# Kernel optimization log

Measured on AMD Instinct MI355X. Metric: run time of the kernel, lower is better.

Reference implementation:

```python
import jax, jax.numpy as jnp
import numpy as np

EPS = 1e-5
LEAK = 0.33  # scn LeakyReLU default leakiness


def leaky(x):
    return jnp.where(x > 0, x, LEAK * x)


def subm_conv(feat, idx, mask, w):
    # feat: [N,C], idx: [N,K] int, mask: [N,K] bool, w: [K,Cin,Cout]
    g = feat[idx] * mask[..., None]          # [N,K,C] gather of active neighbors
    return jnp.einsum('nkc,kcd->nd', g, w)   # [N,Cout]


def batch_norm(x, gamma, beta):
    # scn BatchNormalization in training mode: batch stats over active sites
    m = x.mean(axis=0)
    v = x.var(axis=0)
    return (x - m) * jax.lax.rsqrt(v + EPS) * gamma + beta


def setup_inputs() -> dict:
    key = jax.random.key(0)
    ks = jax.random.split(key, 8)
    N, K, C, B = 131072, 9, 64, 4
    features = jax.random.normal(ks[0], (N, C), dtype=jnp.float32)
    neighbor_idx = jax.random.randint(ks[1], (N, K), 0, N, dtype=jnp.int32)
    # center offset always points at self (submanifold conv semantics)
    neighbor_idx = neighbor_idx.at[:, K // 2].set(jnp.arange(N, dtype=jnp.int32))
    neighbor_mask = jax.random.randint(ks[2], (N, K), 0, 2) > 0
    neighbor_mask = neighbor_mask.at[:, K // 2].set(True)
    scale = 1.0 / np.sqrt(K * C)
    conv1_w = jax.random.normal(ks[3], (B, K, C, C), dtype=jnp.float32) * scale
    conv2_w = jax.random.normal(ks[4], (B, K, C, C), dtype=jnp.float32) * scale
    bn1_gamma = jnp.ones((B, C), dtype=jnp.float32)
    bn1_beta = jnp.zeros((B, C), dtype=jnp.float32)
    bn2_gamma = jnp.ones((B, C), dtype=jnp.float32)
    bn2_beta = jnp.zeros((B, C), dtype=jnp.float32)
    return {
        'features': features, 'neighbor_idx': neighbor_idx, 'neighbor_mask': neighbor_mask,
        'conv1_w': conv1_w, 'bn1_gamma': bn1_gamma, 'bn1_beta': bn1_beta,
        'conv2_w': conv2_w, 'bn2_gamma': bn2_gamma, 'bn2_beta': bn2_beta,
    }


def reference(features, neighbor_idx, neighbor_mask, conv1_w, bn1_gamma, bn1_beta,
              conv2_w, bn2_gamma, bn2_beta):
    x = features
    n_blocks = conv1_w.shape[0]
    for b in range(n_blocks):
        residual = x
        out = subm_conv(x, neighbor_idx, neighbor_mask, conv1_w[b])
        out = leaky(batch_norm(out, bn1_gamma[b], bn1_beta[b]))
        out = subm_conv(out, neighbor_idx, neighbor_mask, conv2_w[b])
        out = batch_norm(out, bn2_gamma[b], bn2_beta[b])
        x = leaky(out + residual)
    return x
```

## Files before the change

kernel.cpp:

```cpp
#include <hip/hip_runtime.h>
#include <hip/hip_bf16.h>
#include <stdint.h>

#define NROWS 131072
#define EPSBN 1e-5f
#define LEAKK 0.33f

typedef __bf16 bf16x8_t __attribute__((ext_vector_type(8)));
typedef float  f32x4_t  __attribute__((ext_vector_type(4)));

__device__ __forceinline__ float leaky_f(float x) { return fmaxf(x, LEAKK * x); }

#define GLDS16(g, l)                                                          \
    __builtin_amdgcn_global_load_lds(                                         \
        (const __attribute__((address_space(1))) void*)(g),                   \
        (__attribute__((address_space(3))) void*)(l), 16, 0, 0)

#define WAIT_VM18 0x4F72
#define WAIT_VM10 0x0F7A
#define WAIT_VM8  0x0F78
#define WAIT_VM0  0x0F70
#define CFENCE() asm volatile("" ::: "memory")

__global__ __launch_bounds__(256, 2) void conv_kernel(
    const __bf16* __restrict__ src,
    const int* __restrict__ cidxT,
    const __bf16* __restrict__ wt,
    __bf16* __restrict__ dst,
    float* __restrict__ stat_out)
{
    __shared__ char Ab[2][32768];
    __shared__ char Bb[2][8192];

    const int tid  = threadIdx.x;
    const int lane = tid & 63;
    const int wv   = tid >> 6;
    const int quad = lane >> 4;
    const int l15  = lane & 15;
    const int row0 = blockIdx.x << 8;
    const int srow = tid >> 3;
    const int cg   = (tid & 7) ^ (srow & 7);
    const int ldsl = (tid & 192) << 4;
    const int sxor = l15 & 7;

    const char* srcb = (const char*)src;
    const char* wtb  = (const char*)wt;

    f32x4_t acc[4][4];
#pragma unroll
    for (int mt = 0; mt < 4; ++mt)
#pragma unroll
        for (int nt = 0; nt < 4; ++nt)
            acc[mt][nt] = (f32x4_t){0.f, 0.f, 0.f, 0.f};

    int ix[2][8];
#pragma unroll
    for (int i = 0; i < 8; ++i) ix[0][i] = cidxT[row0 + (i << 5) + srow];
    CFENCE();
#pragma unroll
    for (int i = 0; i < 8; ++i) ix[1][i] = cidxT[NROWS + row0 + (i << 5) + srow];
    CFENCE();
    __builtin_amdgcn_s_waitcnt(WAIT_VM8);
#pragma unroll
    for (int i = 0; i < 8; ++i)
        GLDS16(srcb + ((size_t)ix[0][i] << 7) + (cg << 4), &Ab[0][(i << 12) + ldsl]);
#pragma unroll
    for (int i = 0; i < 2; ++i)
        GLDS16(wtb + (((i << 5) + srow) << 7) + (cg << 4), &Bb[0][(i << 12) + ldsl]);
    CFENCE();

#pragma unroll
    for (int k = 0; k < 9; ++k) {
        const int cur = k & 1, nxt = cur ^ 1;
        if (k < 7) {
#pragma unroll
            for (int i = 0; i < 8; ++i)
                ix[k & 1][i] = cidxT[(k + 2) * NROWS + row0 + (i << 5) + srow];
        }
        CFENCE();
        if (k < 7)       __builtin_amdgcn_s_waitcnt(WAIT_VM18);
        else if (k == 7) __builtin_amdgcn_s_waitcnt(WAIT_VM10);
        if (k < 8) {
            const int* ixu = ix[(k + 1) & 1];
#pragma unroll
            for (int i = 0; i < 8; ++i)
                GLDS16(srcb + ((size_t)ixu[i] << 7) + (cg << 4),
                       &Ab[nxt][(i << 12) + ldsl]);
#pragma unroll
            for (int i = 0; i < 2; ++i)
                GLDS16(wtb + ((size_t)(k + 1) << 13) + (((i << 5) + srow) << 7) + (cg << 4),
                       &Bb[nxt][(i << 12) + ldsl]);
        }
        CFENCE();
        if (k < 7)       __builtin_amdgcn_s_waitcnt(WAIT_VM18);
        else if (k == 7) __builtin_amdgcn_s_waitcnt(WAIT_VM10);
        else             __builtin_amdgcn_s_waitcnt(WAIT_VM0);
        __builtin_amdgcn_s_barrier();
        bf16x8_t af[4][2], bq[4][2];
#pragma unroll
        for (int ks = 0; ks < 2; ++ks) {
            const int slot = ((quad | (ks << 2)) ^ sxor) << 4;
#pragma unroll
            for (int mt = 0; mt < 4; ++mt) {
                int m = (wv << 6) + (mt << 4) + l15;
                af[mt][ks] = *(const bf16x8_t*)&Ab[cur][(m << 7) + slot];
            }
#pragma unroll
            for (int nt = 0; nt < 4; ++nt) {
                int d = (nt << 4) + l15;
                bq[nt][ks] = *(const bf16x8_t*)&Bb[cur][(d << 7) + slot];
            }
        }
#pragma unroll
        for (int ks = 0; ks < 2; ++ks)
#pragma unroll
            for (int mt = 0; mt < 4; ++mt)
#pragma unroll
                for (int nt = 0; nt < 4; ++nt)
                    acc[mt][nt] = __builtin_amdgcn_mfma_f32_16x16x32_bf16(
                        af[mt][ks], bq[nt][ks], acc[mt][nt], 0, 0, 0);
        __builtin_amdgcn_s_barrier();
    }

#pragma unroll
    for (int mt = 0; mt < 4; ++mt) {
        int rowb = row0 + (wv << 6) + (mt << 4) + (quad << 2);
#pragma unroll
        for (int nt = 0; nt < 4; ++nt) {
            int col = (nt << 4) + l15;
#pragma unroll
            for (int r = 0; r < 4; ++r)
                dst[((size_t)(rowb + r) << 6) + col] = (__bf16)acc[mt][nt][r];
        }
    }
    float* red = (float*)Bb[1];
    __syncthreads();
    if (tid < 128) red[tid] = 0.f;
    __syncthreads();
#pragma unroll
    for (int nt = 0; nt < 4; ++nt) {
        float s = 0.f, q = 0.f;
#pragma unroll
        for (int mt = 0; mt < 4; ++mt)
#pragma unroll
            for (int r = 0; r < 4; ++r) { float v = acc[mt][nt][r]; s += v; q += v * v; }
        s += __shfl_xor(s, 16); s += __shfl_xor(s, 32);
        q += __shfl_xor(q, 16); q += __shfl_xor(q, 32);
        if (lane < 16) {
            atomicAdd(&red[(nt << 4) + lane], s);
            atomicAdd(&red[64 + (nt << 4) + lane], q);
        }
    }
    __syncthreads();
    if (tid < 128) atomicAdd(&stat_out[tid], red[tid]);
}

__global__ __launch_bounds__(256) void bnact_kernel(
    __bf16* __restrict__ y, const float* __restrict__ stat,
    const float* __restrict__ gamma, const float* __restrict__ beta)
{
    __shared__ float sc[64], sh[64];
    int tid = threadIdx.x;
    if (tid < 64) {
        float m = stat[tid] * (1.f / NROWS);
        float v = stat[64 + tid] * (1.f / NROWS) - m * m;
        float s = gamma[tid] * rsqrtf(v + EPSBN);
        sc[tid] = s;
        sh[tid] = beta[tid] - m * s;
    }
    __syncthreads();
    size_t base = ((((size_t)blockIdx.x << 8) | tid) << 3);
    int c0 = (int)(base & 63);
    bf16x8_t hv = *(bf16x8_t*)(y + base);
#pragma unroll
    for (int j = 0; j < 8; ++j) {
        float f = (float)hv[j];
        f = leaky_f(f * sc[c0 + j] + sh[c0 + j]);
        hv[j] = (__bf16)f;
    }
    *(bf16x8_t*)(y + base) = hv;
}

__global__ __launch_bounds__(256) void resid_kernel(
    const __bf16* __restrict__ z, const float* __restrict__ xin,
    float* __restrict__ xf, __bf16* __restrict__ xh, float* __restrict__ dout,
    const float* __restrict__ stat, const float* __restrict__ gamma,
    const float* __restrict__ beta, int isfinal)
{
    __shared__ float sc[64], sh[64];
    int tid = threadIdx.x;
    if (tid < 64) {
        float m = stat[tid] * (1.f / NROWS);
        float v = stat[64 + tid] * (1.f / NROWS) - m * m;
        float s = gamma[tid] * rsqrtf(v + EPSBN);
        sc[tid] = s;
        sh[tid] = beta[tid] - m * s;
    }
    __syncthreads();
    size_t base = ((((size_t)blockIdx.x << 8) | tid) << 3);
    int c0 = (int)(base & 63);
    bf16x8_t zv = *(const bf16x8_t*)(z + base);
    float4 xa = *(const float4*)(xin + base);
    float4 xb = *(const float4*)(xin + base + 4);
    float o[8];
#pragma unroll
    for (int j = 0; j < 8; ++j) {
        float xv = (j < 4) ? (&xa.x)[j] : (&xb.x)[j - 4];
        o[j] = leaky_f((float)zv[j] * sc[c0 + j] + sh[c0 + j] + xv);
    }
    if (isfinal) {
        *(float4*)(dout + base)     = make_float4(o[0], o[1], o[2], o[3]);
        *(float4*)(dout + base + 4) = make_float4(o[4], o[5], o[6], o[7]);
    } else {
        *(float4*)(xf + base)     = make_float4(o[0], o[1], o[2], o[3]);
        *(float4*)(xf + base + 4) = make_float4(o[4], o[5], o[6], o[7]);
        bf16x8_t h;
#pragma unroll
        for (int j = 0; j < 8; ++j) h[j] = (__bf16)o[j];
        *(bf16x8_t*)(xh + base) = h;
    }
}

__global__ __launch_bounds__(256) void prep_kernel(
    const float* __restrict__ feat, const float* __restrict__ w1,
    const float* __restrict__ w2, const int* __restrict__ nidx,
    const unsigned char* __restrict__ mraw,
    __bf16* __restrict__ fh, __bf16* __restrict__ yh,
    __bf16* __restrict__ wtp, int* __restrict__ cidxT,
    float* __restrict__ stats)
{
    size_t t = ((size_t)blockIdx.x << 8) | threadIdx.x;
    if (t < 1024) stats[t] = 0.f;
    if (t < 64) {
        fh[(size_t)NROWS * 64 + t] = (__bf16)0.f;
        yh[(size_t)NROWS * 64 + t] = (__bf16)0.f;
    }
    if (t < 1048576) {
        size_t i = t << 3;
        float4 a = *(const float4*)(feat + i);
        float4 b = *(const float4*)(feat + i + 4);
        bf16x8_t h;
        h[0] = (__bf16)a.x; h[1] = (__bf16)a.y; h[2] = (__bf16)a.z; h[3] = (__bf16)a.w;
        h[4] = (__bf16)b.x; h[5] = (__bf16)b.y; h[6] = (__bf16)b.z; h[7] = (__bf16)b.w;
        *(bf16x8_t*)(fh + i) = h;
    }
    if (t < 294912) {
        int o = (int)t;
        int c = o & 63, d = (o >> 6) & 63;
        int kk = o >> 12;
        int k = kk % 9, bb = (kk / 9) & 3, cv = kk / 36;
        const float* w = cv ? w2 : w1;
        float v = w[((size_t)((bb * 9 + k) * 64 + c) << 6) + d];
        wtp[o] = (__bf16)v;
    }
    if (t < 1179648) {
        int k = (int)(t >> 17), n = (int)(t & 131071);
        bool bytes_enc = (mraw[13] != 0);
        int e = n * 9 + k;
        bool m = bytes_enc ? (mraw[e] != 0) : (((const unsigned int*)mraw)[e] != 0u);
        cidxT[t] = m ? nidx[e] : NROWS;
    }
}

extern "C" void kernel_launch(void* const* d_in, const int* in_sizes, int n_in,
                              void* d_out, int out_size, void* d_ws, size_t ws_size,
                              hipStream_t stream) {
    const float* feat = (const float*)d_in[0];
    const int* nidx = (const int*)d_in[1];
    const unsigned char* mraw = (const unsigned char*)d_in[2];
    const float* w1 = (const float*)d_in[3];
    const float* g1 = (const float*)d_in[4];
    const float* b1 = (const float*)d_in[5];
    const float* w2 = (const float*)d_in[6];
    const float* g2 = (const float*)d_in[7];
    const float* b2 = (const float*)d_in[8];
    float* out = (float*)d_out;

    char* ws = (char*)d_ws;
    float*  xf    = (float*)ws;
    __bf16* xh    = (__bf16*)(ws + 33554432);
    __bf16* yh    = (__bf16*)(ws + 50331904);
    __bf16* zh    = (__bf16*)(ws + 67109376);
    __bf16* wtp   = (__bf16*)(ws + 83886592);
    float*  stats = (float*)(ws + 84476416);
    int*    cidxT = (int*)(ws + 84480512);

    prep_kernel<<<4608, 256, 0, stream>>>(feat, w1, w2, nidx, mraw,
                                          xh, yh, wtp, cidxT, stats);

    for (int b = 0; b < 4; ++b) {
        conv_kernel<<<512, 256, 0, stream>>>(
            xh, cidxT, wtp + (size_t)b * 9 * 4096,
            yh, stats + (size_t)(2 * b) * 128);
        bnact_kernel<<<4096, 256, 0, stream>>>(
            yh, stats + (size_t)(2 * b) * 128, g1 + b * 64, b1 + b * 64);
        conv_kernel<<<512, 256, 0, stream>>>(
            yh, cidxT, wtp + (size_t)(4 + b) * 9 * 4096,
            zh, stats + (size_t)(2 * b + 1) * 128);
        resid_kernel<<<4096, 256, 0, stream>>>(
            zh, (b == 0) ? feat : xf, xf, xh, out,
            stats + (size_t)(2 * b + 1) * 128, g2 + b * 64, b2 + b * 64,
            (b == 3) ? 1 : 0);
    }
}
```

Before: 418.2 us.

## Drop fp32 residual buffer, restructure conv waits, and coalesce index prep

The fp32 residual copy xf is removed, so the residual kernel reads the bf16 activation xh in place and no longer writes fp32 state. This halves residual traffic at the cost of bf16 rounding on the residual path. The conv loop drops the early vmcnt wait before issuing the next gathers and instead adds an lgkm wait before the closing barrier. The prep kernel now handles one row per thread across all 9 offsets, with a smaller grid.

```diff
diff --git a/kernel.cpp b/kernel.cpp
--- a/kernel.cpp
+++ b/kernel.cpp
@@ -16,10 +16,11 @@
         (const __attribute__((address_space(1))) void*)(g),                   \
         (__attribute__((address_space(3))) void*)(l), 16, 0, 0)
 
-#define WAIT_VM18 0x4F72
-#define WAIT_VM10 0x0F7A
-#define WAIT_VM8  0x0F78
-#define WAIT_VM0  0x0F70
+#define WAIT_VM18  0x4F72
+#define WAIT_VM10  0x0F7A
+#define WAIT_VM8   0x0F78
+#define WAIT_VM0   0x0F70
+#define WAIT_LGKM0 0xC07F
 #define CFENCE() asm volatile("" ::: "memory")
 
 __global__ __launch_bounds__(256, 2) void conv_kernel(
@@ -78,8 +79,6 @@
                 ix[k & 1][i] = cidxT[(k + 2) * NROWS + row0 + (i << 5) + srow];
         }
         CFENCE();
-        if (k < 7)       __builtin_amdgcn_s_waitcnt(WAIT_VM18);
-        else if (k == 7) __builtin_amdgcn_s_waitcnt(WAIT_VM10);
         if (k < 8) {
             const int* ixu = ix[(k + 1) & 1];
 #pragma unroll
@@ -119,7 +118,10 @@
                 for (int nt = 0; nt < 4; ++nt)
                     acc[mt][nt] = __builtin_amdgcn_mfma_f32_16x16x32_bf16(
                         af[mt][ks], bq[nt][ks], acc[mt][nt], 0, 0, 0);
+        CFENCE();
+        __builtin_amdgcn_s_waitcnt(WAIT_LGKM0);
         __builtin_amdgcn_s_barrier();
+        CFENCE();
     }
 
 #pragma unroll
@@ -182,10 +184,10 @@
 }
 
 __global__ __launch_bounds__(256) void resid_kernel(
-    const __bf16* __restrict__ z, const float* __restrict__ xin,
-    float* __restrict__ xf, __bf16* __restrict__ xh, float* __restrict__ dout,
+    const __bf16* __restrict__ z, const float* __restrict__ featin,
+    __bf16* __restrict__ xh, float* __restrict__ dout,
     const float* __restrict__ stat, const float* __restrict__ gamma,
-    const float* __restrict__ beta, int isfinal)
+    const float* __restrict__ beta, int isfirst, int isfinal)
 {
     __shared__ float sc[64], sh[64];
     int tid = threadIdx.x;
@@ -200,20 +202,25 @@
     size_t base = ((((size_t)blockIdx.x << 8) | tid) << 3);
     int c0 = (int)(base & 63);
     bf16x8_t zv = *(const bf16x8_t*)(z + base);
-    float4 xa = *(const float4*)(xin + base);
-    float4 xb = *(const float4*)(xin + base + 4);
+    float xv[8];
+    if (isfirst) {
+        float4 xa = *(const float4*)(featin + base);
+        float4 xb = *(const float4*)(featin + base + 4);
+#pragma unroll
+        for (int j = 0; j < 4; ++j) { xv[j] = (&xa.x)[j]; xv[4 + j] = (&xb.x)[j]; }
+    } else {
+        bf16x8_t xr = *(const bf16x8_t*)(xh + base);
+#pragma unroll
+        for (int j = 0; j < 8; ++j) xv[j] = (float)xr[j];
+    }
     float o[8];
 #pragma unroll
-    for (int j = 0; j < 8; ++j) {
-        float xv = (j < 4) ? (&xa.x)[j] : (&xb.x)[j - 4];
-        o[j] = leaky_f((float)zv[j] * sc[c0 + j] + sh[c0 + j] + xv);
-    }
+    for (int j = 0; j < 8; ++j)
+        o[j] = leaky_f((float)zv[j] * sc[c0 + j] + sh[c0 + j] + xv[j]);
     if (isfinal) {
         *(float4*)(dout + base)     = make_float4(o[0], o[1], o[2], o[3]);
         *(float4*)(dout + base + 4) = make_float4(o[4], o[5], o[6], o[7]);
     } else {
-        *(float4*)(xf + base)     = make_float4(o[0], o[1], o[2], o[3]);
-        *(float4*)(xf + base + 4) = make_float4(o[4], o[5], o[6], o[7]);
         bf16x8_t h;
 #pragma unroll
         for (int j = 0; j < 8; ++j) h[j] = (__bf16)o[j];
@@ -253,12 +260,16 @@
         float v = w[((size_t)((bb * 9 + k) * 64 + c) << 6) + d];
         wtp[o] = (__bf16)v;
     }
-    if (t < 1179648) {
-        int k = (int)(t >> 17), n = (int)(t & 131071);
-        bool bytes_enc = (mraw[13] != 0);
-        int e = n * 9 + k;
-        bool m = bytes_enc ? (mraw[e] != 0) : (((const unsigned int*)mraw)[e] != 0u);
-        cidxT[t] = m ? nidx[e] : NROWS;
+    if (t < NROWS) {
+        int n = (int)t;
+        bool benc = (mraw[13] != 0);
+        const unsigned int* mw = (const unsigned int*)mraw;
+#pragma unroll
+        for (int j = 0; j < 9; ++j) {
+            int e = n * 9 + j;
+            bool m = benc ? (mraw[e] != 0) : (mw[e] != 0u);
+            cidxT[j * NROWS + n] = m ? nidx[e] : NROWS;
+        }
     }
 }
 
@@ -277,15 +288,14 @@
     float* out = (float*)d_out;
 
     char* ws = (char*)d_ws;
-    float*  xf    = (float*)ws;
-    __bf16* xh    = (__bf16*)(ws + 33554432);
-    __bf16* yh    = (__bf16*)(ws + 50331904);
-    __bf16* zh    = (__bf16*)(ws + 67109376);
-    __bf16* wtp   = (__bf16*)(ws + 83886592);
-    float*  stats = (float*)(ws + 84476416);
-    int*    cidxT = (int*)(ws + 84480512);
-
-    prep_kernel<<<4608, 256, 0, stream>>>(feat, w1, w2, nidx, mraw,
+    __bf16* xh    = (__bf16*)ws;
+    __bf16* yh    = (__bf16*)(ws + 17825792);
+    __bf16* zh    = (__bf16*)(ws + 35651584);
+    __bf16* wtp   = (__bf16*)(ws + 53477376);
+    float*  stats = (float*)(ws + 54525952);
+    int*    cidxT = (int*)(ws + 54591488);
+
+    prep_kernel<<<4096, 256, 0, stream>>>(feat, w1, w2, nidx, mraw,
                                           xh, yh, wtp, cidxT, stats);
 
     for (int b = 0; b < 4; ++b) {
@@ -298,8 +308,8 @@
             yh, cidxT, wtp + (size_t)(4 + b) * 9 * 4096,
             zh, stats + (size_t)(2 * b + 1) * 128);
         resid_kernel<<<4096, 256, 0, stream>>>(
-            zh, (b == 0) ? feat : xf, xf, xh, out,
+            zh, feat, xh, out,
             stats + (size_t)(2 * b + 1) * 128, g2 + b * 64, b2 + b * 64,
-            (b == 3) ? 1 : 0);
-    }
-}
+            (b == 0) ? 1 : 0, (b == 3) ? 1 : 0);
+    }
+}
```

Result: faster. 400.7 us (-4.2%).
